# Kernel optimization log

Hardware: AMD Instinct MI355X
Metric: run time of the kernel (lower is better)

The kernel has to match this reference:

```python
import jax, jax.numpy as jnp
import numpy as np

LN_EPS = 1e-5
COS_EPS2 = 1e-16  # torch cosine_similarity: (n1*n2).clamp_min(eps**2), eps=1e-8


def _ln(x, g, b):
    m = jnp.mean(x, -1, keepdims=True)
    v = jnp.mean((x - m) ** 2, -1, keepdims=True)
    return (x - m) * jax.lax.rsqrt(v + LN_EPS) * g + b


def _span_pool(x, starts, ends, word_length):
    # x: [B, S, D] (text_feat[:, 1:]); spans pooled into slots 1..S of a [B, S+1, D] buffer
    B, S, D = x.shape
    cs = jnp.concatenate([jnp.zeros((B, 1, D), x.dtype), jnp.cumsum(x, axis=1)], axis=1)  # [B, S+1, D]
    pool = (jnp.take_along_axis(cs, ends[..., None], axis=1)
            - jnp.take_along_axis(cs, starts[..., None], axis=1))  # [B, S, D]
    mask = (jnp.arange(S)[None, :] < word_length[:, None]).astype(x.dtype)[..., None]
    return jnp.pad(pool * mask, ((0, 0), (1, 0), (0, 0)))  # [B, S+1, D], slot 0 = zeros


def _forward(text_hidden, vit_feature, pooler_out, target_mask, adj,
             ln_g, ln_b, wq, wk, wv, fc_w, mha_ln_g, mha_ln_b,
             w1a, b1a, w1b, b1b, w2a, b2a, w2b, b2b,
             loc_w, loc_b, out_w, out_b, word_length, tran_indices):
    B, L, D = text_hidden.shape
    H = wq.shape[1] // D  # n_head=4, d_k=d_v=768

    # eval mode: all dropouts are identity
    text_feat = _ln(text_hidden, ln_g, ln_b)

    # MultiHeadAttention(text_feat, vit, vit)
    q = (text_feat @ wq).reshape(B, L, H, D)
    k = (vit_feature @ wk).reshape(B, -1, H, D)
    v = (vit_feature @ wv).reshape(B, -1, H, D)
    attn = jnp.einsum('blhd,bmhd->bhlm', q, k) / jnp.sqrt(jnp.asarray(D, text_feat.dtype))
    attn = jax.nn.softmax(attn, axis=-1)
    ctx = jnp.einsum('bhlm,bmhd->blhd', attn, v).reshape(B, L, H * D)
    text_include_img = _ln(ctx @ fc_w + text_feat, mha_ln_g, mha_ln_b)

    # pairwise cosine similarity over sequence positions: [B, L, L]
    n = jnp.linalg.norm(text_include_img, axis=-1)
    sim = jnp.einsum('bld,bmd->blm', text_include_img, text_include_img)
    sim = sim / jnp.maximum(n[:, :, None] * n[:, None, :], COS_EPS2)

    global_bert = _ln(pooler_out, ln_g, ln_b)

    # span pooling of subword features into word slots (tmps buffers)
    starts, ends = tran_indices[..., 0], tran_indices[..., 1]
    tmps = _span_pool(text_feat[:, 1:, :], starts, ends, word_length)
    tmps_ti = _span_pool(text_include_img[:, 1:, :], starts, ends, word_length)

    adj_ti = adj * sim
    den = jnp.sum(adj, axis=2, keepdims=True) + 1.0
    den_ti = jnp.sum(adj_ti, axis=2, keepdims=True) + 1.0

    # NOTE: original loop recomputes from tmps each layer and only keeps the last
    # iteration, so only W1[-1]/W2[-1] affect the output (faithfully reproduced).
    g_dep = jax.nn.relu(((adj @ tmps) @ w1b + b1b) / den)
    g_ti = jax.nn.relu(((adj_ti @ tmps_ti) @ w2b + b2b) / den_ti)

    asp_wn = jnp.sum(target_mask, axis=1, keepdims=True)  # [B, 1]
    m = target_mask[:, :, None]
    gcn_out_text = jnp.sum(g_dep * m, axis=1) / asp_wn
    gcn_out_ti = jnp.sum(g_ti * m, axis=1) / asp_wn

    local_feat = jnp.concatenate([gcn_out_text, gcn_out_ti], axis=1) @ loc_w + loc_b
    feat = jnp.concatenate([global_bert, local_feat], axis=1)
    return feat @ out_w + out_b


def setup_inputs():
    key = jax.random.key(0)
    ks = jax.random.split(key, 20)
    B, L, NV, D, H, NC = 64, 160, 197, 768, 4, 3
    S = L - 1
    s = 0.02
    text_hidden = jax.random.normal(ks[0], (B, L, D), jnp.float32)
    vit_feature = jax.random.normal(ks[1], (B, NV, D), jnp.float32)
    pooler_out = jax.random.normal(ks[2], (B, D), jnp.float32)
    adj = jax.random.uniform(ks[3], (B, L, L), jnp.float32)
    target_mask = jnp.zeros((B, L), jnp.float32).at[:, 1:9].set(1.0)
    word_length = jax.random.randint(ks[4], (B,), 1, S, jnp.int32)
    lens = jax.random.randint(ks[5], (B, S), 1, 3, jnp.int32)  # 1-2 subtokens per word
    cum = jnp.cumsum(lens, axis=1)
    ends = jnp.minimum(cum, S)
    starts = jnp.minimum(cum - lens, S)
    tran_indices = jnp.stack([starts, ends], axis=-1).astype(jnp.int32)
    return dict(
        text_hidden=text_hidden, vit_feature=vit_feature, pooler_out=pooler_out,
        target_mask=target_mask, adj=adj,
        ln_g=jnp.ones((D,), jnp.float32), ln_b=jnp.zeros((D,), jnp.float32),
        wq=jax.random.normal(ks[6], (D, H * D), jnp.float32) * s,
        wk=jax.random.normal(ks[7], (D, H * D), jnp.float32) * s,
        wv=jax.random.normal(ks[8], (D, H * D), jnp.float32) * s,
        fc_w=jax.random.normal(ks[9], (H * D, D), jnp.float32) * s,
        mha_ln_g=jnp.ones((D,), jnp.float32), mha_ln_b=jnp.zeros((D,), jnp.float32),
        w1a=jax.random.normal(ks[10], (D, D), jnp.float32) * s, b1a=jnp.zeros((D,), jnp.float32),
        w1b=jax.random.normal(ks[11], (D, D), jnp.float32) * s, b1b=jnp.zeros((D,), jnp.float32),
        w2a=jax.random.normal(ks[12], (D, D), jnp.float32) * s, b2a=jnp.zeros((D,), jnp.float32),
        w2b=jax.random.normal(ks[13], (D, D), jnp.float32) * s, b2b=jnp.zeros((D,), jnp.float32),
        loc_w=jax.random.normal(ks[14], (2 * D, D), jnp.float32) * s, loc_b=jnp.zeros((D,), jnp.float32),
        out_w=jax.random.normal(ks[15], (2 * D, NC), jnp.float32) * s, out_b=jnp.zeros((NC,), jnp.float32),
        word_length=word_length, tran_indices=tran_indices,
    )


def reference(text_hidden, vit_feature, pooler_out, target_mask, adj,
              ln_g, ln_b, wq, wk, wv, fc_w, mha_ln_g, mha_ln_b,
              w1a, b1a, w1b, b1b, w2a, b2a, w2b, b2b,
              loc_w, loc_b, out_w, out_b, word_length, tran_indices):
    return _forward(text_hidden, vit_feature, pooler_out, target_mask, adj,
                    ln_g, ln_b, wq, wk, wv, fc_w, mha_ln_g, mha_ln_b,
                    w1a, b1a, w1b, b1b, w2a, b2a, w2b, b2b,
                    loc_w, loc_b, out_w, out_b, word_length, tran_indices)
```

## Files before the change

kernel.cpp:

```cpp
#include <hip/hip_runtime.h>
#include <math.h>

#define BB 64
#define LL 160
#define DD 768
#define HH 4
#define NVV 197
#define SS 159

typedef unsigned short u16;
typedef __attribute__((ext_vector_type(8))) short bf16x8;
typedef __attribute__((ext_vector_type(4))) float f32x4;

union QU { uint4 u; bf16x8 v; };

__device__ __forceinline__ u16 f2bf(float a) {
  unsigned u = __builtin_bit_cast(unsigned, a);
  u = (u + 0x7FFFu + ((u >> 16) & 1u)) >> 16;
  return (u16)u;
}
__device__ __forceinline__ unsigned f2bf2(float a, float b) {
  return (unsigned)f2bf(a) | ((unsigned)f2bf(b) << 16);
}
__device__ __forceinline__ float bf2f(u16 h) {
  unsigned u = ((unsigned)h) << 16;
  return __builtin_bit_cast(float, u);
}
__device__ __forceinline__ float to_f(float x) { return x; }
__device__ __forceinline__ float to_f(u16 x) { return bf2f(x); }

__device__ __forceinline__ void async16(const u16* g, void* l) {
  __builtin_amdgcn_global_load_lds(
      (const __attribute__((address_space(1))) void*)g,
      (__attribute__((address_space(3))) void*)l, 16, 0, 0);
}

__device__ __forceinline__ uint4 load_bf8(const u16* __restrict__ P, long long rowbase,
                                          int valid, int kb, int K) {
  uint4 r;
  if (valid && (kb + 8 <= K) && (((rowbase + kb) & 7) == 0)) {
    r = *(const uint4*)(P + rowbase + kb);
  } else {
    u16 e[8];
    #pragma unroll
    for (int i = 0; i < 8; ++i) { int k = kb + i; e[i] = (valid && k < K) ? P[rowbase + k] : (u16)0; }
    r.x = e[0] | ((unsigned)e[1] << 16); r.y = e[2] | ((unsigned)e[3] << 16);
    r.z = e[4] | ((unsigned)e[5] << 16); r.w = e[6] | ((unsigned)e[7] << 16);
  }
  return r;
}

__device__ __forceinline__ uint4 load_row8(const float* __restrict__ P, long long rowbase,
                                           int valid_row, int kb, int K) {
  float f[8];
  if (valid_row && (kb + 8 <= K)) {
    const float4* p0 = (const float4*)(P + rowbase + kb);
    float4 x = p0[0], y = p0[1];
    f[0] = x.x; f[1] = x.y; f[2] = x.z; f[3] = x.w;
    f[4] = y.x; f[5] = y.y; f[6] = y.z; f[7] = y.w;
  } else {
    #pragma unroll
    for (int e = 0; e < 8; ++e) { int k = kb + e; f[e] = (valid_row && k < K) ? P[rowbase + k] : 0.f; }
  }
  uint4 r;
  r.x = f2bf2(f[0], f[1]); r.y = f2bf2(f[2], f[3]);
  r.z = f2bf2(f[4], f[5]); r.w = f2bf2(f[6], f[7]);
  return r;
}

__device__ __forceinline__ uint4 load_a(const u16* P, long long rb, int v, int kb, int K) {
  return load_bf8(P, rb, v, kb, K);
}
__device__ __forceinline__ uint4 load_a(const float* P, long long rb, int v, int kb, int K) {
  return load_row8(P, rb, v, kb, K);
}

template<int BMH, int DUAL>
__global__ __launch_bounds__(512) void gemm_ph(
    const u16* __restrict__ A0, const u16* __restrict__ B0m,
    float* __restrict__ Cf0, u16* __restrict__ Cb0,
    const u16* __restrict__ A1, const u16* __restrict__ B1m,
    float* __restrict__ Cf1, u16* __restrict__ Cb1,
    int M, int N, int K, int lda, int ldb, int ldc, int nbx,
    const float* __restrict__ bias0, const float* __restrict__ bias1,
    const u16* __restrict__ resid0,
    const float* __restrict__ rowdiv0, const float* __restrict__ rowdiv1,
    int relu) {
  constexpr int BM = BMH ? 128 : 256;
  constexpr int MR = BMH ? 4 : 8;

  __shared__ uint4 Al[2][4][BM];
  __shared__ uint4 Bl[2][4][128];

  int id = blockIdx.x;
  int nset = gridDim.x >> DUAL;
  int setid = DUAL ? (id >= nset ? 1 : 0) : 0;
  if (setid) id -= nset;
  const u16* A = setid ? A1 : A0;
  const u16* Bm = setid ? B1m : B0m;
  float* Cf = setid ? Cf1 : Cf0;
  u16* Cb = setid ? Cb1 : Cb0;
  const float* bias = setid ? bias1 : bias0;
  const float* rowdiv = setid ? rowdiv1 : rowdiv0;
  const u16* residB = setid ? (const u16*)nullptr : resid0;

  int qq = nset >> 3, rr = nset & 7;
  int xcd = id & 7, idx = id >> 3;
  int swz = (xcd < rr ? xcd * (qq + 1) : rr * (qq + 1) + (xcd - rr) * qq) + idx;
  int bx = swz % nbx, by = swz / nbx;
  int row0 = by * BM, col0 = bx * 128;

  int t = threadIdx.x, l = t & 63, w = t >> 6;
  int wm = w >> 2, wn = w & 3;
  int li = l & 15, kg = l >> 4;
  int nt = K >> 5;
  int wks = w & 3;
  int wrg = (w >> 2) * 64;

  f32x4 acc[MR][2] = {};

  auto STAGE = [&](int kt, int bi) {
    long long ko = ((long long)kt << 5) + wks * 8;
    async16(Bm + (long long)(col0 + wrg + l) * ldb + ko, &Bl[bi][wks][wrg]);
    async16(A + (long long)(row0 + wrg + l) * lda + ko, &Al[bi][wks][wrg]);
    if (BM == 256)
      async16(A + (long long)(row0 + 128 + wrg + l) * lda + ko, &Al[bi][wks][128 + wrg]);
  };

  STAGE(0, 0);
  __syncthreads();
  int buf = 0;
  for (int kt = 0; kt < nt; ++kt) {
    if (kt + 1 < nt) STAGE(kt + 1, buf ^ 1);
    QU bF[2], aF[MR];
    bF[0].u = Bl[buf][kg][wn * 32 + li];
    bF[1].u = Bl[buf][kg][wn * 32 + 16 + li];
    #pragma unroll
    for (int m = 0; m < MR; ++m)
      aF[m].u = Al[buf][kg][wm * (MR * 16) + m * 16 + li];
    __builtin_amdgcn_s_setprio(1);
    #pragma unroll
    for (int m = 0; m < MR; ++m) {
      acc[m][0] = __builtin_amdgcn_mfma_f32_16x16x32_bf16(aF[m].v, bF[0].v, acc[m][0], 0, 0, 0);
      acc[m][1] = __builtin_amdgcn_mfma_f32_16x16x32_bf16(aF[m].v, bF[1].v, acc[m][1], 0, 0, 0);
    }
    __builtin_amdgcn_s_setprio(0);
    __syncthreads();
    buf ^= 1;
  }

  #pragma unroll
  for (int m = 0; m < MR; ++m)
    #pragma unroll
    for (int n = 0; n < 2; ++n) {
      int col = col0 + wn * 32 + n * 16 + li;
      float bv = bias ? bias[col] : 0.f;
      #pragma unroll
      for (int r = 0; r < 4; ++r) {
        int row = row0 + wm * (MR * 16) + m * 16 + kg * 4 + r;
        long long ci = (long long)row * ldc + col;
        float v = acc[m][n][r] + bv;
        if (residB) v += bf2f(residB[ci]);
        if (rowdiv) v /= rowdiv[row];
        if (relu) v = fmaxf(v, 0.f);
        if (Cf) Cf[ci] = v;
        if (Cb) Cb[ci] = f2bf(v);
      }
    }
}

template<bool TRANSB, typename TA>
__global__ __launch_bounds__(256) void gemm_bf16(
    const TA* __restrict__ A, const u16* __restrict__ Bm,
    float* __restrict__ Cf, u16* __restrict__ Cb,
    int M, int N, int K, int lda, int ldb, int ldc, int Hb,
    long long sAb, long long sAh, long long sBb, long long sBh,
    long long sCb, long long sCh,
    float alpha, const float* __restrict__ bias) {
  int bb = blockIdx.z / Hb, hh = blockIdx.z % Hb;
  A += bb * sAb + hh * sAh;
  Bm += bb * sBb + hh * sBh;
  long long coff = bb * sCb + hh * sCh;

  __shared__ uint4 As4[4][64];
  __shared__ uint4 Bs4[4][64];

  int row0 = blockIdx.y * 64, col0 = blockIdx.x * 64;
  int t = threadIdx.x;
  int l = t & 63, w = t >> 6;
  int mq = (w >> 1) * 32, nq = (w & 1) * 32;

  int am = t >> 2, akq = t & 3;
  int bn = t & 63, bkq = t >> 6;

  f32x4 acc[2][2] = {};

  for (int k0 = 0; k0 < K; k0 += 32) {
    As4[akq][am] = load_a(A, (long long)(row0 + am) * lda, (row0 + am) < M, k0 + akq * 8, K);
    if (TRANSB) {
      Bs4[akq][am] = load_bf8(Bm, (long long)(col0 + am) * ldb, (col0 + am) < N, k0 + akq * 8, K);
    } else {
      int gn = col0 + bn;
      u16 e[8];
      #pragma unroll
      for (int i = 0; i < 8; ++i) {
        int k = k0 + bkq * 8 + i;
        e[i] = (gn < N && k < K) ? Bm[(long long)k * ldb + gn] : (u16)0;
      }
      uint4 r;
      r.x = e[0] | ((unsigned)e[1] << 16); r.y = e[2] | ((unsigned)e[3] << 16);
      r.z = e[4] | ((unsigned)e[5] << 16); r.w = e[6] | ((unsigned)e[7] << 16);
      Bs4[bkq][bn] = r;
    }
    __syncthreads();
    int kg = l >> 4, li = l & 15;
    QU a0, a1, b0, b1;
    a0.u = As4[kg][mq + li];
    a1.u = As4[kg][mq + 16 + li];
    b0.u = Bs4[kg][nq + li];
    b1.u = Bs4[kg][nq + 16 + li];
    acc[0][0] = __builtin_amdgcn_mfma_f32_16x16x32_bf16(a0.v, b0.v, acc[0][0], 0, 0, 0);
    acc[0][1] = __builtin_amdgcn_mfma_f32_16x16x32_bf16(a0.v, b1.v, acc[0][1], 0, 0, 0);
    acc[1][0] = __builtin_amdgcn_mfma_f32_16x16x32_bf16(a1.v, b0.v, acc[1][0], 0, 0, 0);
    acc[1][1] = __builtin_amdgcn_mfma_f32_16x16x32_bf16(a1.v, b1.v, acc[1][1], 0, 0, 0);
    __syncthreads();
  }

  #pragma unroll
  for (int i = 0; i < 2; ++i) {
    #pragma unroll
    for (int j = 0; j < 2; ++j) {
      int colj = col0 + nq + j * 16 + (l & 15);
      float bv = (bias && colj < N) ? bias[colj] : 0.f;
      #pragma unroll
      for (int r = 0; r < 4; ++r) {
        int gr = row0 + mq + i * 16 + (l >> 4) * 4 + r;
        if (gr < M && colj < N) {
          long long ci = coff + (long long)gr * ldc + colj;
          float v = acc[i][j][r] * alpha + bv;
          if (Cf) Cf[ci] = v;
          if (Cb) Cb[ci] = f2bf(v);
        }
      }
    }
  }
}

__global__ __launch_bounds__(256) void sim_kernel(
    const u16* __restrict__ TII, const float* __restrict__ nrm,
    const u16* __restrict__ adjB, u16* __restrict__ adjtiB) {
  int bb = blockIdx.z;
  const u16* T = TII + (long long)bb * LL * DD;

  __shared__ uint4 As4[4][64];
  __shared__ uint4 Bs4[4][64];

  int row0 = blockIdx.y * 64, col0 = blockIdx.x * 64;
  int t = threadIdx.x;
  int l = t & 63, w = t >> 6;
  int mq = (w >> 1) * 32, nq = (w & 1) * 32;
  int am = t >> 2, akq = t & 3;

  f32x4 acc[2][2] = {};

  for (int k0 = 0; k0 < DD; k0 += 32) {
    As4[akq][am] = load_bf8(T, (long long)(row0 + am) * DD, (row0 + am) < LL, k0 + akq * 8, DD);
    Bs4[akq][am] = load_bf8(T, (long long)(col0 + am) * DD, (col0 + am) < LL, k0 + akq * 8, DD);
    __syncthreads();
    int kg = l >> 4, li = l & 15;
    QU a0, a1, b0, b1;
    a0.u = As4[kg][mq + li];
    a1.u = As4[kg][mq + 16 + li];
    b0.u = Bs4[kg][nq + li];
    b1.u = Bs4[kg][nq + 16 + li];
    acc[0][0] = __builtin_amdgcn_mfma_f32_16x16x32_bf16(a0.v, b0.v, acc[0][0], 0, 0, 0);
    acc[0][1] = __builtin_amdgcn_mfma_f32_16x16x32_bf16(a0.v, b1.v, acc[0][1], 0, 0, 0);
    acc[1][0] = __builtin_amdgcn_mfma_f32_16x16x32_bf16(a1.v, b0.v, acc[1][0], 0, 0, 0);
    acc[1][1] = __builtin_amdgcn_mfma_f32_16x16x32_bf16(a1.v, b1.v, acc[1][1], 0, 0, 0);
    __syncthreads();
  }

  #pragma unroll
  for (int i = 0; i < 2; ++i) {
    #pragma unroll
    for (int j = 0; j < 2; ++j) {
      int colj = col0 + nq + j * 16 + (l & 15);
      #pragma unroll
      for (int r = 0; r < 4; ++r) {
        int gr = row0 + mq + i * 16 + (l >> 4) * 4 + r;
        if (gr < LL && colj < LL) {
          float nl = nrm[bb * LL + gr], nm = nrm[bb * LL + colj];
          long long ai = ((long long)bb * LL + gr) * LL + colj;
          float s = acc[i][j][r] / fmaxf(nl * nm, 1e-16f);
          adjtiB[ai] = f2bf(bf2f(adjB[ai]) * s);
        }
      }
    }
  }
}

__device__ __forceinline__ float block_sum(float v, float* sm) {
  #pragma unroll
  for (int o = 32; o > 0; o >>= 1) v += __shfl_down(v, o);
  int lane = threadIdx.x & 63, w = threadIdx.x >> 6;
  if (lane == 0) sm[w] = v;
  __syncthreads();
  if (threadIdx.x == 0) sm[0] = sm[0] + sm[1] + sm[2] + sm[3];
  __syncthreads();
  float r = sm[0];
  __syncthreads();
  return r;
}

__global__ __launch_bounds__(256) void ln_kernel(const float* __restrict__ x, float* __restrict__ yf,
                                                 u16* __restrict__ yb,
                                                 const float* __restrict__ g, const float* __restrict__ b,
                                                 float* __restrict__ nrmout) {
  __shared__ float sm[4];
  long long row = blockIdx.x;
  const float* xr = x + row * DD;
  int t = threadIdx.x;
  float v0 = xr[t], v1 = xr[t + 256], v2 = xr[t + 512];
  float s = block_sum(v0 + v1 + v2, sm);
  float m = s * (1.f / 768.f);
  float d0 = v0 - m, d1 = v1 - m, d2 = v2 - m;
  float vv = block_sum(d0 * d0 + d1 * d1 + d2 * d2, sm);
  float rstd = rsqrtf(vv * (1.f / 768.f) + 1e-5f);
  float y0 = d0 * rstd * g[t] + b[t];
  float y1 = d1 * rstd * g[t + 256] + b[t + 256];
  float y2 = d2 * rstd * g[t + 512] + b[t + 512];
  if (yf) { float* yr = yf + row * DD; yr[t] = y0; yr[t + 256] = y1; yr[t + 512] = y2; }
  if (yb) { u16* yr = yb + row * DD; yr[t] = f2bf(y0); yr[t + 256] = f2bf(y1); yr[t + 512] = f2bf(y2); }
  if (nrmout) {
    float s2 = block_sum(y0 * y0 + y1 * y1 + y2 * y2, sm);
    if (t == 0) nrmout[row] = sqrtf(s2);
  }
}

__global__ __launch_bounds__(256) void softmax_bf16(u16* __restrict__ SP, int nrows) {
  int row = blockIdx.x * 4 + (threadIdx.x >> 6);
  int lane = threadIdx.x & 63;
  if (row >= nrows) return;
  u16* ar = SP + (long long)row * 200;
  float vals[4];
  float mx = -1e30f;
  int cnt = 0;
  for (int i = lane; i < NVV; i += 64) { float v = bf2f(ar[i]); vals[cnt++] = v; mx = fmaxf(mx, v); }
  #pragma unroll
  for (int o = 32; o > 0; o >>= 1) mx = fmaxf(mx, __shfl_xor(mx, o));
  float sum = 0.f;
  for (int j = 0; j < cnt; ++j) { vals[j] = __expf(vals[j] - mx); sum += vals[j]; }
  #pragma unroll
  for (int o = 32; o > 0; o >>= 1) sum += __shfl_xor(sum, o);
  float inv = 1.f / sum;
  cnt = 0;
  for (int i = lane; i < NVV; i += 64) ar[i] = f2bf(vals[cnt++] * inv);
  for (int i = NVV + lane; i < 200; i += 64) ar[i] = 0;
}

template<typename T>
__global__ __launch_bounds__(256) void pool_kernel(const T* __restrict__ src, u16* __restrict__ dst,
                                                   const int* __restrict__ wl, const int* __restrict__ tran) {
  int b = blockIdx.x, i = blockIdx.y, d = threadIdx.x;
  long long ob = ((long long)b * LL + i) * DD;
  float r0 = 0.f, r1 = 0.f, r2 = 0.f;
  if (i > 0 && (i - 1) < wl[b]) {
    int w = i - 1;
    int st = tran[(b * SS + w) * 2];
    int en = tran[(b * SS + w) * 2 + 1];
    const T* sb = src + (long long)b * LL * DD;
    for (int s = st; s < en; ++s) {
      const T* rp = sb + (long long)(1 + s) * DD;
      r0 += to_f(rp[d]); r1 += to_f(rp[d + 256]); r2 += to_f(rp[d + 512]);
    }
  }
  dst[ob + d] = f2bf(r0);
  dst[ob + d + 256] = f2bf(r1);
  dst[ob + d + 512] = f2bf(r2);
}

__global__ __launch_bounds__(256) void adjconv_den(const float* __restrict__ adjf, u16* __restrict__ adjB,
                                                   float* __restrict__ den) {
  __shared__ float sm[4];
  int bl = blockIdx.x, m = threadIdx.x;
  float a = 0.f;
  if (m < LL) {
    long long idx = (long long)bl * LL + m;
    a = adjf[idx];
    adjB[idx] = f2bf(a);
  }
  float sa = block_sum(a, sm);
  if (m == 0) den[bl] = sa + 1.f;
}

__global__ __launch_bounds__(256) void denti_kernel(const u16* __restrict__ atB, float* __restrict__ den_ti) {
  __shared__ float sm[4];
  int bl = blockIdx.x, m = threadIdx.x;
  float at = 0.f;
  if (m < LL) at = bf2f(atB[(long long)bl * LL + m]);
  float sat = block_sum(at, sm);
  if (m == 0) den_ti[bl] = sat + 1.f;
}

__global__ __launch_bounds__(256) void gcn_kernel(const u16* __restrict__ g, const float* __restrict__ mask,
                                                  u16* __restrict__ outB, int coloff) {
  int b = blockIdx.x;
  int d = blockIdx.y * 256 + threadIdx.x;
  float s = 0.f, wn = 0.f;
  for (int l = 0; l < LL; ++l) {
    float mk = mask[b * LL + l];
    wn += mk;
    s += mk * bf2f(g[((long long)b * LL + l) * DD + d]);
  }
  outB[(long long)b * (2 * DD) + coloff + d] = f2bf(s / wn);
}

__global__ __launch_bounds__(256) void final_kernel(const float* __restrict__ gb, const float* __restrict__ lf,
                                                    const float* __restrict__ ow, const float* __restrict__ ob,
                                                    float* __restrict__ out) {
  __shared__ float sm[4];
  int b = blockIdx.x / 3, c = blockIdx.x % 3;
  int t = threadIdx.x;
  float s = 0.f;
  for (int k = t; k < DD; k += 256) {
    s += gb[b * DD + k] * ow[k * 3 + c];
    s += lf[b * DD + k] * ow[(DD + k) * 3 + c];
  }
  float tot = block_sum(s, sm);
  if (t == 0) out[b * 3 + c] = tot + ob[c];
}

__global__ __launch_bounds__(256) void conv_kernel(const float4* __restrict__ x, uint2* __restrict__ y, int n4) {
  int i = blockIdx.x * 256 + threadIdx.x;
  if (i < n4) {
    float4 v = x[i];
    uint2 o;
    o.x = f2bf2(v.x, v.y);
    o.y = f2bf2(v.z, v.w);
    y[i] = o;
  }
}

__global__ __launch_bounds__(256) void tconv_kernel(const float* __restrict__ src, u16* __restrict__ dst,
                                                    int R, int C, int lds, int ldd) {
  __shared__ float sm[32][33];
  int t = threadIdx.x;
  int tx = t & 31, ty8 = t >> 5;
  int r0 = blockIdx.y * 32, c0 = blockIdx.x * 32;
  for (int i = ty8; i < 32; i += 8) {
    int r = r0 + i, c = c0 + tx;
    sm[i][tx] = (r < R && c < C) ? src[(long long)r * lds + c] : 0.f;
  }
  __syncthreads();
  for (int i = ty8; i < 32; i += 8) {
    int c = c0 + i, r = r0 + tx;
    if (c < C && r < R) dst[(long long)c * ldd + r] = f2bf(sm[tx][i]);
  }
}

__global__ __launch_bounds__(256) void vtrans_kernel(const u16* __restrict__ src, u16* __restrict__ dst) {
  __shared__ u16 sm[32][33];
  int b = blockIdx.z;
  int c0 = blockIdx.x * 32;
  int r0 = blockIdx.y * 32;
  int t = threadIdx.x, tx = t & 31, ty8 = t >> 5;
  const u16* sb = src + (long long)b * NVV * DD;
  for (int i = ty8; i < 32; i += 8) {
    int r = r0 + i, c = c0 + tx;
    sm[i][tx] = (r < NVV && c < DD) ? sb[(long long)r * DD + c] : (u16)0;
  }
  __syncthreads();
  u16* db = dst + (long long)b * DD * 208;
  for (int i = ty8; i < 32; i += 8) {
    int j = c0 + i, k = r0 + tx;
    if (j < DD && k < 208) db[(long long)j * 208 + k] = sm[tx][i];
  }
}

template<typename TA>
static void gemm(hipStream_t s, bool transb, const TA* A, const u16* B, float* Cf, u16* Cb,
                 int M, int N, int K, int lda, int ldb, int ldc, int batches, int Hb,
                 long long sAb, long long sAh, long long sBb, long long sBh,
                 long long sCb, long long sCh, float alpha, const float* bias) {
  dim3 g((N + 63) / 64, (M + 63) / 64, batches);
  if (transb)
    gemm_bf16<true, TA><<<g, 256, 0, s>>>(A, B, Cf, Cb, M, N, K, lda, ldb, ldc, Hb,
                                          sAb, sAh, sBb, sBh, sCb, sCh, alpha, bias);
  else
    gemm_bf16<false, TA><<<g, 256, 0, s>>>(A, B, Cf, Cb, M, N, K, lda, ldb, ldc, Hb,
                                           sAb, sAh, sBb, sBh, sCb, sCh, alpha, bias);
}

extern "C" void kernel_launch(void* const* d_in, const int* in_sizes, int n_in,
                              void* d_out, int out_size, void* d_ws, size_t ws_size,
                              hipStream_t stream) {
  const float* text_hidden = (const float*)d_in[0];
  const float* vit_feature = (const float*)d_in[1];
  const float* pooler_out = (const float*)d_in[2];
  const float* target_mask = (const float*)d_in[3];
  const float* adj = (const float*)d_in[4];
  const float* ln_g = (const float*)d_in[5];
  const float* ln_b = (const float*)d_in[6];
  const float* wq = (const float*)d_in[7];
  const float* wk = (const float*)d_in[8];
  const float* wv = (const float*)d_in[9];
  const float* fc_w = (const float*)d_in[10];
  const float* mha_ln_g = (const float*)d_in[11];
  const float* mha_ln_b = (const float*)d_in[12];
  const float* w1b = (const float*)d_in[15];
  const float* b1b = (const float*)d_in[16];
  const float* w2b = (const float*)d_in[19];
  const float* b2b = (const float*)d_in[20];
  const float* loc_w = (const float*)d_in[21];
  const float* loc_b = (const float*)d_in[22];
  const float* out_w = (const float*)d_in[23];
  const float* out_b = (const float*)d_in[24];
  const int* word_length = (const int*)d_in[25];
  const int* tran = (const int*)d_in[26];
  float* out = (float*)d_out;

  const long long BLD = (long long)BB * LL * DD;
  const long long BND = (long long)BB * NVV * DD;
  const long long WHD = (long long)768 * 768;
  const long long W3K = (long long)768 * 3072;

  char* base = (char*)d_ws;
  auto alloc = [&](size_t bytes) { char* p = base; base += (bytes + 255) & ~(size_t)255; return p; };

  float* R_ACC = (float*)alloc(BLD * 4);
  u16* TFB = (u16*)alloc(BLD * 2);
  u16* vitB = (u16*)alloc(BND * 2);
  u16* BIG = (u16*)alloc((size_t)4 * BLD * 2);
  u16* Mt = (u16*)alloc((size_t)4 * WHD * 2);
  u16* Wvf = (u16*)alloc((size_t)4 * WHD * 2);
  u16* SH = (u16*)alloc((size_t)BB * HH * LL * 200 * 2);
  u16* adjtiB = (u16*)alloc((size_t)BB * LL * LL * 2);
  u16* adjB = (u16*)alloc((size_t)BB * LL * LL * 2);
  u16* w1bT = (u16*)alloc(WHD * 2);
  u16* w2bT = (u16*)alloc(WHD * 2);
  u16* locT = (u16*)alloc((size_t)768 * 1536 * 2);
  u16* linB = (u16*)alloc((size_t)BB * 1536 * 2);
  float* nrm = (float*)alloc((size_t)BB * LL * 4);
  float* den = (float*)alloc((size_t)BB * LL * 4);
  float* den_ti = (float*)alloc((size_t)BB * LL * 4);
  float* global_bert = (float*)alloc((size_t)BB * DD * 4);
  float* local_feat = (float*)alloc((size_t)BB * DD * 4);

  u16* wqB = BIG;
  u16* wkB = BIG + W3K;
  u16* wvB = BIG + 2 * W3K;
  u16* fcT = BIG + 3 * W3K;
  u16* T2PV = BIG;
  u16* TIIB = BIG + 2 * BLD;
  u16* tmpsTiB = BIG;
  u16* g2B = BIG + BLD;
  u16* S4 = SH;
  u16* H1 = SH;
  u16* tmpsB = vitB;
  u16* h2B = TFB;
  u16* g1B = vitB;
  u16* vitT = (u16*)R_ACC;

  const float inv_sqrt_d = 1.0f / sqrtf((float)DD);
  const long long sA_L = (long long)LL * DD;

  {
    int n4v = (int)(BND / 4);
    conv_kernel<<<(n4v + 255) / 256, 256, 0, stream>>>((const float4*)vit_feature, (uint2*)vitB, n4v);
    vtrans_kernel<<<dim3(24, 7, BB), 256, 0, stream>>>(vitB, vitT);
    adjconv_den<<<BB * LL, 256, 0, stream>>>(adj, adjB, den);
    int n4w = (int)(W3K / 4);
    conv_kernel<<<(n4w + 255) / 256, 256, 0, stream>>>((const float4*)wq, (uint2*)wqB, n4w);
    conv_kernel<<<(n4w + 255) / 256, 256, 0, stream>>>((const float4*)wk, (uint2*)wkB, n4w);
    conv_kernel<<<(n4w + 255) / 256, 256, 0, stream>>>((const float4*)wv, (uint2*)wvB, n4w);
    for (int h = 0; h < HH; ++h)
      tconv_kernel<<<dim3(24, 24), 256, 0, stream>>>(fc_w + (size_t)h * WHD, fcT + (size_t)h * WHD,
                                                     768, 768, 768, 768);
    tconv_kernel<<<dim3(24, 24), 256, 0, stream>>>(w1b, w1bT, 768, 768, 768, 768);
    tconv_kernel<<<dim3(24, 24), 256, 0, stream>>>(w2b, w2bT, 768, 768, 768, 768);
    tconv_kernel<<<dim3(24, 48), 256, 0, stream>>>(loc_w, locT, 1536, 768, 768, 1536);
    gemm<u16>(stream, true, wkB, wqB, nullptr, Mt, 768, 768, 768, 3072, 3072, 768,
              HH, 1, 768, 0, 768, 0, WHD, 0, 1.f, nullptr);
    gemm<u16>(stream, true, fcT, wvB, nullptr, Wvf, 768, 768, 768, 768, 3072, 3072,
              HH, 1, WHD, 0, 768, 0, 768, 0, 1.f, nullptr);
  }

  ln_kernel<<<BB * LL, 256, 0, stream>>>(text_hidden, nullptr, TFB, ln_g, ln_b, nullptr);
  gemm_ph<0, 0><<<960, 512, 0, stream>>>(TFB, Mt, nullptr, T2PV,
                                         nullptr, nullptr, nullptr, nullptr,
                                         BB * LL, 4 * DD, DD, DD, DD, 4 * DD, 24,
                                         nullptr, nullptr, nullptr, nullptr, nullptr, 0);
  gemm<u16>(stream, true, T2PV, vitB, nullptr, S4, LL, NVV, DD, 4 * DD, DD, 200,
            BB * HH, HH, (long long)LL * 4 * DD, DD, (long long)NVV * DD, 0,
            (long long)HH * LL * 200, (long long)LL * 200, inv_sqrt_d, nullptr);
  softmax_bf16<<<(BB * HH * LL + 3) / 4, 256, 0, stream>>>(S4, BB * HH * LL);
  gemm<u16>(stream, true, S4, vitT, nullptr, T2PV, LL, DD, NVV, 200, 208, 4 * DD,
            BB * HH, HH, (long long)HH * LL * 200, (long long)LL * 200,
            (long long)DD * 208, 0, (long long)LL * 4 * DD, DD, 1.f, nullptr);
  gemm_ph<1, 0><<<480, 512, 0, stream>>>(T2PV, Wvf, R_ACC, nullptr,
                                         nullptr, nullptr, nullptr, nullptr,
                                         BB * LL, DD, 4 * DD, 4 * DD, 4 * DD, DD, 6,
                                         nullptr, nullptr, TFB, nullptr, nullptr, 0);

  ln_kernel<<<BB * LL, 256, 0, stream>>>(R_ACC, nullptr, TIIB, mha_ln_g, mha_ln_b, nrm);
  sim_kernel<<<dim3(3, 3, BB), 256, 0, stream>>>(TIIB, nrm, adjB, adjtiB);
  denti_kernel<<<BB * LL, 256, 0, stream>>>(adjtiB, den_ti);
  pool_kernel<u16><<<dim3(BB, LL), 256, 0, stream>>>(TFB, tmpsB, word_length, tran);
  pool_kernel<u16><<<dim3(BB, LL), 256, 0, stream>>>(TIIB, tmpsTiB, word_length, tran);
  gemm<u16>(stream, false, adjB, tmpsB, nullptr, H1, LL, DD, LL, LL, DD, DD,
            BB, 1, (long long)LL * LL, 0, sA_L, 0, sA_L, 0, 1.f, nullptr);
  gemm<u16>(stream, false, adjtiB, tmpsTiB, nullptr, h2B, LL, DD, LL, LL, DD, DD,
            BB, 1, (long long)LL * LL, 0, sA_L, 0, sA_L, 0, 1.f, nullptr);
  gemm_ph<1, 1><<<960, 512, 0, stream>>>(H1, w1bT, nullptr, g1B,
                                         h2B, w2bT, nullptr, g2B,
                                         BB * LL, DD, DD, DD, DD, DD, 6,
                                         b1b, b2b, nullptr, den, den_ti, 1);
  gcn_kernel<<<dim3(BB, 3), 256, 0, stream>>>(g1B, target_mask, linB, 0);
  gcn_kernel<<<dim3(BB, 3), 256, 0, stream>>>(g2B, target_mask, linB, DD);
  ln_kernel<<<BB, 256, 0, stream>>>(pooler_out, global_bert, nullptr, ln_g, ln_b, nullptr);
  gemm<u16>(stream, true, linB, locT, local_feat, nullptr, BB, DD, 2 * DD, 2 * DD, 2 * DD, DD,
            1, 1, 0, 0, 0, 0, 0, 0, 1.f, loc_b);
  final_kernel<<<BB * 3, 256, 0, stream>>>(global_bert, local_feat, out_w, out_b, out);
}
```

Before: 718.6 us.

## Add 128x128 double-buffered async-copy GEMM for attention and weight-fold matmuls

New measurement: 747.3 us. 1.04x slower.

```diff
diff --git a/kernel.cpp b/kernel.cpp
--- a/kernel.cpp
+++ b/kernel.cpp
@@ -7,6 +7,7 @@
 #define HH 4
 #define NVV 197
 #define SS 159
+#define KP 224
 
 typedef unsigned short u16;
 typedef __attribute__((ext_vector_type(8))) short bf16x8;
@@ -165,6 +166,84 @@
         if (relu) v = fmaxf(v, 0.f);
         if (Cf) Cf[ci] = v;
         if (Cb) Cb[ci] = f2bf(v);
+      }
+    }
+}
+
+__global__ __launch_bounds__(256) void gemm97b(
+    const u16* __restrict__ A, const u16* __restrict__ Bm,
+    float* __restrict__ Cf, u16* __restrict__ Cb,
+    int M, int N, int K, int lda, int ldb, int ldc, int Hb,
+    long long sAb, long long sAh, long long sBb, long long sBh,
+    long long sCb, long long sCh, float alpha) {
+  __shared__ uint4 Al[2][4][128];
+  __shared__ uint4 Bl[2][4][128];
+
+  int z = blockIdx.z, bb = z / Hb, hh = z % Hb;
+  A += bb * sAb + hh * sAh;
+  Bm += bb * sBb + hh * sBh;
+  long long coff = bb * sCb + hh * sCh;
+
+  int row0 = blockIdx.y * 128, col0 = blockIdx.x * 128;
+  int t = threadIdx.x, l = t & 63, w = t >> 6;
+  int wr = (w >> 1) * 64, wc = (w & 1) * 64;
+  int li = l & 15, kg = l >> 4;
+  int nt = K >> 5;
+
+  int ra0 = row0 + l;       if (ra0 > M - 1) ra0 = M - 1;
+  int ra1 = row0 + 64 + l;  if (ra1 > M - 1) ra1 = M - 1;
+  int rb0 = col0 + l;       if (rb0 > N - 1) rb0 = N - 1;
+  int rb1 = col0 + 64 + l;  if (rb1 > N - 1) rb1 = N - 1;
+  const u16* Ap0 = A + (long long)ra0 * lda + w * 8;
+  const u16* Ap1 = A + (long long)ra1 * lda + w * 8;
+  const u16* Bp0 = Bm + (long long)rb0 * ldb + w * 8;
+  const u16* Bp1 = Bm + (long long)rb1 * ldb + w * 8;
+
+  f32x4 acc[4][4] = {};
+
+  auto STAGE = [&](int kt, int bi) {
+    long long ko = (long long)kt << 5;
+    async16(Ap0 + ko, &Al[bi][w][0]);
+    async16(Ap1 + ko, &Al[bi][w][64]);
+    async16(Bp0 + ko, &Bl[bi][w][0]);
+    async16(Bp1 + ko, &Bl[bi][w][64]);
+  };
+
+  STAGE(0, 0);
+  __syncthreads();
+  int buf = 0;
+  for (int kt = 0; kt < nt; ++kt) {
+    if (kt + 1 < nt) STAGE(kt + 1, buf ^ 1);
+    QU a[4], b[4];
+    #pragma unroll
+    for (int i = 0; i < 4; ++i) a[i].u = Al[buf][kg][wr + i * 16 + li];
+    #pragma unroll
+    for (int j = 0; j < 4; ++j) b[j].u = Bl[buf][kg][wc + j * 16 + li];
+    __builtin_amdgcn_s_setprio(1);
+    #pragma unroll
+    for (int i = 0; i < 4; ++i)
+      #pragma unroll
+      for (int j = 0; j < 4; ++j)
+        acc[i][j] = __builtin_amdgcn_mfma_f32_16x16x32_bf16(a[i].v, b[j].v, acc[i][j], 0, 0, 0);
+    __builtin_amdgcn_s_setprio(0);
+    __syncthreads();
+    buf ^= 1;
+  }
+
+  #pragma unroll
+  for (int i = 0; i < 4; ++i)
+    #pragma unroll
+    for (int j = 0; j < 4; ++j) {
+      int col = col0 + wc + j * 16 + li;
+      #pragma unroll
+      for (int r = 0; r < 4; ++r) {
+        int row = row0 + wr + i * 16 + kg * 4 + r;
+        if (row < M && col < N) {
+          long long ci = coff + (long long)row * ldc + col;
+          float v = acc[i][j][r] * alpha;
+          if (Cf) Cf[ci] = v;
+          if (Cb) Cb[ci] = f2bf(v);
+        }
       }
     }
 }
@@ -341,7 +420,7 @@
   int row = blockIdx.x * 4 + (threadIdx.x >> 6);
   int lane = threadIdx.x & 63;
   if (row >= nrows) return;
-  u16* ar = SP + (long long)row * 200;
+  u16* ar = SP + (long long)row * KP;
   float vals[4];
   float mx = -1e30f;
   int cnt = 0;
@@ -355,7 +434,7 @@
   float inv = 1.f / sum;
   cnt = 0;
   for (int i = lane; i < NVV; i += 64) ar[i] = f2bf(vals[cnt++] * inv);
-  for (int i = NVV + lane; i < 200; i += 64) ar[i] = 0;
+  for (int i = NVV + lane; i < KP; i += 64) ar[i] = 0;
 }
 
 template<typename T>
@@ -470,10 +549,10 @@
     sm[i][tx] = (r < NVV && c < DD) ? sb[(long long)r * DD + c] : (u16)0;
   }
   __syncthreads();
-  u16* db = dst + (long long)b * DD * 208;
+  u16* db = dst + (long long)b * DD * KP;
   for (int i = ty8; i < 32; i += 8) {
     int j = c0 + i, k = r0 + tx;
-    if (j < DD && k < 208) db[(long long)j * 208 + k] = sm[tx][i];
+    if (j < DD && k < KP) db[(long long)j * KP + k] = sm[tx][i];
   }
 }
 
@@ -489,6 +568,15 @@
   else
     gemm_bf16<false, TA><<<g, 256, 0, s>>>(A, B, Cf, Cb, M, N, K, lda, ldb, ldc, Hb,
                                            sAb, sAh, sBb, sBh, sCb, sCh, alpha, bias);
+}
+
+static void gemm97bh(hipStream_t s, const u16* A, const u16* B, float* Cf, u16* Cb,
+                     int M, int N, int K, int lda, int ldb, int ldc, int batches, int Hb,
+                     long long sAb, long long sAh, long long sBb, long long sBh,
+                     long long sCb, long long sCh, float alpha) {
+  dim3 g((N + 127) / 128, (M + 127) / 128, batches);
+  gemm97b<<<g, 256, 0, s>>>(A, B, Cf, Cb, M, N, K, lda, ldb, ldc, Hb,
+                            sAb, sAh, sBb, sBh, sCb, sCh, alpha);
 }
 
 extern "C" void kernel_launch(void* const* d_in, const int* in_sizes, int n_in,
@@ -533,7 +621,7 @@
   u16* BIG = (u16*)alloc((size_t)4 * BLD * 2);
   u16* Mt = (u16*)alloc((size_t)4 * WHD * 2);
   u16* Wvf = (u16*)alloc((size_t)4 * WHD * 2);
-  u16* SH = (u16*)alloc((size_t)BB * HH * LL * 200 * 2);
+  u16* SH = (u16*)alloc((size_t)BB * HH * LL * KP * 2);
   u16* adjtiB = (u16*)alloc((size_t)BB * LL * LL * 2);
   u16* adjB = (u16*)alloc((size_t)BB * LL * LL * 2);
   u16* w1bT = (u16*)alloc(WHD * 2);
@@ -579,10 +667,10 @@
     tconv_kernel<<<dim3(24, 24), 256, 0, stream>>>(w1b, w1bT, 768, 768, 768, 768);
     tconv_kernel<<<dim3(24, 24), 256, 0, stream>>>(w2b, w2bT, 768, 768, 768, 768);
     tconv_kernel<<<dim3(24, 48), 256, 0, stream>>>(loc_w, locT, 1536, 768, 768, 1536);
-    gemm<u16>(stream, true, wkB, wqB, nullptr, Mt, 768, 768, 768, 3072, 3072, 768,
-              HH, 1, 768, 0, 768, 0, WHD, 0, 1.f, nullptr);
-    gemm<u16>(stream, true, fcT, wvB, nullptr, Wvf, 768, 768, 768, 768, 3072, 3072,
-              HH, 1, WHD, 0, 768, 0, 768, 0, 1.f, nullptr);
+    gemm97bh(stream, wkB, wqB, nullptr, Mt, 768, 768, 768, 3072, 3072, 768,
+             HH, HH, 0, 768, 0, 768, 0, WHD, 1.f);
+    gemm97bh(stream, fcT, wvB, nullptr, Wvf, 768, 768, 768, 768, 3072, 3072,
+             HH, HH, 0, WHD, 0, 768, 0, 768, 1.f);
   }
 
   ln_kernel<<<BB * LL, 256, 0, stream>>>(text_hidden, nullptr, TFB, ln_g, ln_b, nullptr);
@@ -590,13 +678,13 @@
                                          nullptr, nullptr, nullptr, nullptr,
                                          BB * LL, 4 * DD, DD, DD, DD, 4 * DD, 24,
                                          nullptr, nullptr, nullptr, nullptr, nullptr, 0);
-  gemm<u16>(stream, true, T2PV, vitB, nullptr, S4, LL, NVV, DD, 4 * DD, DD, 200,
-            BB * HH, HH, (long long)LL * 4 * DD, DD, (long long)NVV * DD, 0,
-            (long long)HH * LL * 200, (long long)LL * 200, inv_sqrt_d, nullptr);
+  gemm97bh(stream, T2PV, vitB, nullptr, S4, LL, NVV, DD, 4 * DD, DD, KP,
+           BB * HH, HH, (long long)LL * 4 * DD, DD, (long long)NVV * DD, 0,
+           (long long)HH * LL * KP, (long long)LL * KP, inv_sqrt_d);
   softmax_bf16<<<(BB * HH * LL + 3) / 4, 256, 0, stream>>>(S4, BB * HH * LL);
-  gemm<u16>(stream, true, S4, vitT, nullptr, T2PV, LL, DD, NVV, 200, 208, 4 * DD,
-            BB * HH, HH, (long long)HH * LL * 200, (long long)LL * 200,
-            (long long)DD * 208, 0, (long long)LL * 4 * DD, DD, 1.f, nullptr);
+  gemm97bh(stream, S4, vitT, nullptr, T2PV, LL, DD, KP, KP, KP, 4 * DD,
+           BB * HH, HH, (long long)HH * LL * KP, (long long)LL * KP,
+           (long long)DD * KP, 0, (long long)LL * 4 * DD, DD, 1.f);
   gemm_ph<1, 0><<<480, 512, 0, stream>>>(T2PV, Wvf, R_ACC, nullptr,
                                          nullptr, nullptr, nullptr, nullptr,
                                          BB * LL, DD, 4 * DD, 4 * DD, 4 * DD, DD, 6,
```
